# Optimization experiments

Hardware: AMD Instinct MI355X
Metric: run time of the kernel (lower is better)

The kernel has to match this reference:

```python
import jax, jax.numpy as jnp
import numpy as np

B, L, D = 4, 1024, 256
H, HD, W = 8, 64, 3


def setup_inputs() -> dict:
    key = jax.random.key(0)
    ks = jax.random.split(key, 5)
    return {
        'x': jax.random.normal(ks[0], (B, L, D), dtype=jnp.float32),
        'Wq': jax.random.normal(ks[1], (D, H * HD), dtype=jnp.float32) * 0.05,
        'bq': jnp.zeros((H, 1, 1, HD), dtype=jnp.float32),
        'Wk': jax.random.normal(ks[2], (D, H * HD), dtype=jnp.float32) * 0.05,
        'bk': jnp.zeros((H, 1, 1, HD), dtype=jnp.float32),
        'Wv': jax.random.normal(ks[3], (D, H), dtype=jnp.float32) * 0.05,
        'pe': jax.random.normal(ks[4], (L, D), dtype=jnp.float32) * 0.05,
    }


def reference(x, Wq, bq, Wk, bk, Wv, pe):
    b, l, d = x.shape
    h, hd = bq.shape[0], bq.shape[-1]
    xpe = x + pe  # learned positional encoding added for Q and K only
    # tf.split over axis 3 into h heads + concat axis 0 == reshape then head-major transpose
    q = (xpe @ Wq).reshape(b, l, h, hd).transpose(2, 0, 1, 3) + bq  # [H,B,L,hd]
    k = (xpe @ Wk).reshape(b, l, h, hd).transpose(2, 0, 1, 3) + bk  # [H,B,L,hd]
    v = jax.nn.sigmoid(x @ Wv).transpose(2, 0, 1)  # [H,B,L]
    att = jnp.einsum('hbqd,hbkd->hbqk', q, k) / jnp.sqrt(jnp.asarray(hd, x.dtype))
    att = jax.nn.softmax(att, axis=-1)  # [H,B,L,L]
    # band_part(0,-1) + diag_part(k=(0,L-1)) + transpose + reverse(-2,-1) is
    # equivalent to: out[.., jp, dist] = att[.., n-dist, n] with n = L-1-jp, masked n-dist>=0
    jp = jnp.arange(l)
    n = l - 1 - jp                      # reversed position index, [L]
    m = n[:, None] - jp[None, :]        # row (query) index per (pos, distance), [L,L]
    valid = m >= 0
    g = att[:, :, jnp.clip(m, 0), n[:, None]]  # gather diagonals -> [H,B,L,L]
    a = jnp.where(valid, g, jnp.asarray(0, x.dtype)) * v[:, :, :, None]
    # avg pool over the distance (last) axis, window W, stride 1, SAME,
    # TF AvgPool excludes padding from the count
    ssum = jax.lax.reduce_window(a, 0.0, jax.lax.add, (1, 1, 1, W), (1, 1, 1, 1), 'SAME')
    cnt = jax.lax.reduce_window(jnp.ones((l,), a.dtype), 0.0, jax.lax.add, (W,), (1,), 'SAME')
    a = ssum / cnt  # [H,B,L,L]
    # global_mode: permute to [B, pos, dist, H] and sum over positions
    return a.transpose(1, 2, 3, 0).sum(axis=1)  # [B, L, H]
```

## Files before the change

kernel.cpp:

```cpp
#include <hip/hip_runtime.h>
#include <hip/hip_bf16.h>
#include <math.h>

#define B 4
#define L 1024
#define D 256
#define H 8
#define HD 64

#define KB_OFF  1048576
#define VR_OFF  2097152
#define TP_OFF  (VR_OFF + 32768)
#define XP_OFF  (TP_OFF + 1048576)
#define WT_OFF  (XP_OFF + 524288)

typedef short short8 __attribute__((ext_vector_type(8)));
typedef float f32x16 __attribute__((ext_vector_type(16)));

__device__ __forceinline__ unsigned short f2bf(float f) {
  __hip_bfloat16 h = __float2bfloat16(f);
  return *reinterpret_cast<unsigned short*>(&h);
}

__global__ __launch_bounds__(256) void prep_wx_kernel(
    const float* __restrict__ x, const float* __restrict__ Wq,
    const float* __restrict__ Wk, const float* __restrict__ Wv,
    const float* __restrict__ pe, float* __restrict__ ws)
{
  const int tid = threadIdx.x;
  if (blockIdx.x < 32) {
    __shared__ float lds[32][257];
    const int c0 = blockIdx.x * 32;
    const float* W = (c0 < 512) ? Wq : Wk;
    const int cc = c0 & 511;
    const int c = tid & 31, dd = tid >> 5;
    for (int d0 = 0; d0 < 256; d0 += 8)
      lds[c][d0 + dd] = W[(d0 + dd) * 512 + cc + c];
    __syncthreads();
    __hip_bfloat16* WT = (__hip_bfloat16*)(ws + WT_OFF);
    for (int cl = 0; cl < 32; ++cl)
      WT[(c0 + cl) * 256 + tid] = __float2bfloat16(lds[cl][tid]);
    return;
  }

  __shared__ float xs[8][257];
  const int r0 = (blockIdx.x - 32) * 8;
  __hip_bfloat16* XP = (__hip_bfloat16*)(ws + XP_OFF);
  for (int idx = tid; idx < 2048; idx += 256) {
    int rr = idx >> 8, c = idx & 255;
    int gr = r0 + rr, l = gr & 1023;
    float xv = x[gr * 256 + c];
    xs[rr][c] = xv;
    XP[gr * 256 + c] = __float2bfloat16(xv + pe[l * 256 + c]);
  }
  __syncthreads();
  {
    int rr = tid >> 5, h = (tid >> 2) & 7, t4 = tid & 3;
    float acc = 0.f;
    const int d0 = t4 << 6;
#pragma unroll 16
    for (int d = 0; d < 64; ++d) acc += xs[rr][d0 + d] * Wv[(d0 + d) * 8 + h];
    acc += __shfl_down(acc, 1, 4);
    acc += __shfl_down(acc, 2, 4);
    if (t4 == 0) {
      float v = 1.f / (1.f + __expf(-acc));
      int gr = r0 + rr;
      int b = gr >> 10, l = gr & 1023;
      ws[VR_OFF + (h * 4 + b) * 1024 + (1023 - l)] = v;
    }
  }
}

__global__ __launch_bounds__(256) void qkgemm_kernel(float* __restrict__ ws,
    const float* __restrict__ bq, const float* __restrict__ bk)
{
  const int tid = threadIdx.x;
  const int w = tid >> 6, lane = tid & 63;
  const int wid = blockIdx.x * 4 + w;
  const int lt = wid & 127;
  const int cp = wid >> 7;

  const __hip_bfloat16* XP = (const __hip_bfloat16*)(ws + XP_OFF);
  const __hip_bfloat16* WT = (const __hip_bfloat16*)(ws + WT_OFF);

  const int ln = (lt << 5) + (lane & 31);
  const int dlo = (lane >> 5) << 3;
  const int ca = (cp << 6) + (lane & 31);
  const __hip_bfloat16* xr = XP + ln * 256 + dlo;
  const __hip_bfloat16* ar = WT + ca * 256 + dlo;
  const __hip_bfloat16* br = ar + (32 * 256);

  f32x16 acca = {0.f,0.f,0.f,0.f,0.f,0.f,0.f,0.f,0.f,0.f,0.f,0.f,0.f,0.f,0.f,0.f};
  f32x16 accb = {0.f,0.f,0.f,0.f,0.f,0.f,0.f,0.f,0.f,0.f,0.f,0.f,0.f,0.f,0.f,0.f};
#pragma unroll
  for (int k = 0; k < 16; ++k) {
    short8 bf  = *(const short8*)(xr + k * 16);
    short8 afa = *(const short8*)(ar + k * 16);
    short8 afb = *(const short8*)(br + k * 16);
    acca = __builtin_amdgcn_mfma_f32_32x32x16_bf16(afa, bf, acca, 0, 0, 0);
    accb = __builtin_amdgcn_mfma_f32_32x32x16_bf16(afb, bf, accb, 0, 0, 0);
  }

  const int b = ln >> 10, l = ln & 1023;
  const int hq = cp & 7;
  const int hi4 = (lane >> 5) << 2;
  const float* bias = (cp < 8) ? bq : bk;
  const int cbase = hq << 6;
  __hip_bfloat16* base = (__hip_bfloat16*)ws + ((cp < 8) ? 0 : (size_t)KB_OFF * 2);
  __hip_bfloat16* dst = base + ((((size_t)(hq * 4 + b) << 10) + l) << 6);

#pragma unroll
  for (int q = 0; q < 4; ++q) {
    int hd0 = (q << 3) + hi4;
    float4 bv = *(const float4*)(bias + cbase + hd0);
    ushort4 pk;
    pk.x = f2bf(acca[4 * q + 0] + bv.x);
    pk.y = f2bf(acca[4 * q + 1] + bv.y);
    pk.z = f2bf(acca[4 * q + 2] + bv.z);
    pk.w = f2bf(acca[4 * q + 3] + bv.w);
    *(ushort4*)(dst + hd0) = pk;

    int hd1 = hd0 + 32;
    float4 bw = *(const float4*)(bias + cbase + hd1);
    ushort4 pk2;
    pk2.x = f2bf(accb[4 * q + 0] + bw.x);
    pk2.y = f2bf(accb[4 * q + 1] + bw.y);
    pk2.z = f2bf(accb[4 * q + 2] + bw.z);
    pk2.w = f2bf(accb[4 * q + 3] + bw.w);
    *(ushort4*)(dst + hd1) = pk2;
  }
}

__global__ __launch_bounds__(256) void attn_kernel(float* __restrict__ ws)
{
  __shared__ float V[4][64][17];
  __shared__ float Tb[4][1056];
  __shared__ float smerge[4][32];
  const int tid = threadIdx.x;
  const int w = tid >> 6, lane = tid & 63;
  const int i = blockIdx.x;
  const int hb = i & 31;
  const int qt = i >> 5;

  for (int idx = tid; idx < 4 * 1056; idx += 256) (&Tb[0][0])[idx] = 0.f;

  const __hip_bfloat16* Qb = (const __hip_bfloat16*)ws + ((size_t)hb << 16);
  const __hip_bfloat16* Kb = (const __hip_bfloat16*)(ws + KB_OFF) + ((size_t)hb << 16);
  const float* __restrict__ vr = ws + VR_OFF + (hb << 10);

  const int qrow = (qt << 5) + (lane & 31);
  const int dlo = (lane >> 5) << 3;
  const int coff = (lane >> 5) << 2;

  const __hip_bfloat16* qr = Qb + (qrow << 6) + dlo;
  short8 qf0 = *(const short8*)(qr);
  short8 qf1 = *(const short8*)(qr + 16);
  short8 qf2 = *(const short8*)(qr + 32);
  short8 qf3 = *(const short8*)(qr + 48);

#define GLOADK(kt, kf)                                                        \
  {                                                                           \
    const __hip_bfloat16* kr_ = Kb + ((((kt) << 5) + (lane & 31)) << 6) + dlo;\
    kf[0] = *(const short8*)(kr_);                                            \
    kf[1] = *(const short8*)(kr_ + 16);                                       \
    kf[2] = *(const short8*)(kr_ + 32);                                       \
    kf[3] = *(const short8*)(kr_ + 48);                                       \
  }

  float sp0 = 0.f, sp1 = 0.f, sp2 = 0.f, sp3 = 0.f;
#pragma unroll
  for (int t = 0; t < 2; ++t) {
    const int kt0 = w + (t << 2);
    short8 kA[4], kB[4], kC[4], kD[4];
    GLOADK(kt0, kA);
    GLOADK(kt0 + 8, kB);
    GLOADK(kt0 + 16, kC);
    GLOADK(kt0 + 24, kD);
    f32x16 aA = {0.f,0.f,0.f,0.f,0.f,0.f,0.f,0.f,0.f,0.f,0.f,0.f,0.f,0.f,0.f,0.f};
    f32x16 aB = {0.f,0.f,0.f,0.f,0.f,0.f,0.f,0.f,0.f,0.f,0.f,0.f,0.f,0.f,0.f,0.f};
    f32x16 aC = {0.f,0.f,0.f,0.f,0.f,0.f,0.f,0.f,0.f,0.f,0.f,0.f,0.f,0.f,0.f,0.f};
    f32x16 aD = {0.f,0.f,0.f,0.f,0.f,0.f,0.f,0.f,0.f,0.f,0.f,0.f,0.f,0.f,0.f,0.f};
#pragma unroll
    for (int s = 0; s < 4; ++s) {
      short8 qs = (s == 0) ? qf0 : (s == 1) ? qf1 : (s == 2) ? qf2 : qf3;
      aA = __builtin_amdgcn_mfma_f32_32x32x16_bf16(kA[s], qs, aA, 0, 0, 0);
      aB = __builtin_amdgcn_mfma_f32_32x32x16_bf16(kB[s], qs, aB, 0, 0, 0);
      aC = __builtin_amdgcn_mfma_f32_32x32x16_bf16(kC[s], qs, aC, 0, 0, 0);
      aD = __builtin_amdgcn_mfma_f32_32x32x16_bf16(kD[s], qs, aD, 0, 0, 0);
    }
#pragma unroll
    for (int r = 0; r < 16; ++r) {
      sp0 += __expf(aA[r] * 0.125f);
      sp1 += __expf(aB[r] * 0.125f);
      sp2 += __expf(aC[r] * 0.125f);
      sp3 += __expf(aD[r] * 0.125f);
    }
  }
  float s_part = (sp0 + sp1) + (sp2 + sp3);
  s_part += __shfl_xor(s_part, 32);
  if (lane < 32) smerge[w][lane] = s_part;
  __syncthreads();
  const int q = lane & 31;
  const float inv = 1.f / (smerge[0][q] + smerge[1][q] + smerge[2][q] + smerge[3][q]);

#define FLUSH(dt_, acc_)                                                      \
  {                                                                           \
    const int kt_ = qt + (dt_);                                               \
    const float* vb_ = vr + (kt_ << 5) + coff;                                \
    float4 v0_ = *(const float4*)(vb_);                                       \
    float4 v1_ = *(const float4*)(vb_ + 8);                                   \
    float4 v2_ = *(const float4*)(vb_ + 16);                                  \
    float4 v3_ = *(const float4*)(vb_ + 24);                                  \
    _Pragma("unroll")                                                         \
    for (int r = 0; r < 16; ++r) {                                            \
      float vv_ = (r < 4) ? (&v0_.x)[r] : (r < 8) ? (&v1_.x)[r - 4]           \
                : (r < 12) ? (&v2_.x)[r - 8] : (&v3_.x)[r - 12];              \
      V[w][lane][r] = __expf(acc_[r] * 0.125f) * vv_ * inv;                   \
    }                                                                         \
    float accg_ = 0.f;                                                        \
    _Pragma("unroll")                                                         \
    for (int hi = 0; hi < 2; ++hi)                                            \
      _Pragma("unroll")                                                       \
      for (int r = 0; r < 16; ++r) {                                          \
        int l_ = (hi << 2) + (r & 3) + ((r >> 2) << 3) + 31 - lane;           \
        if (l_ >= 0 && l_ < 32) accg_ += V[w][(hi << 5) + l_][r];             \
      }                                                                       \
    Tb[w][((dt_) << 5) + lane] = accg_;                                       \
  }

  const int dtmax = 31 - qt;
  for (int dt = w; dt <= dtmax; dt += 8) {
    const int dt2 = dt + 4;
    const bool has2 = (dt2 <= dtmax);
    const int kta = qt + dt;
    const int ktb = qt + (has2 ? dt2 : dt);
    short8 ka[4], kb[4];
    GLOADK(kta, ka);
    GLOADK(ktb, kb);
    f32x16 acca = {0.f,0.f,0.f,0.f,0.f,0.f,0.f,0.f,0.f,0.f,0.f,0.f,0.f,0.f,0.f,0.f};
    f32x16 accb = {0.f,0.f,0.f,0.f,0.f,0.f,0.f,0.f,0.f,0.f,0.f,0.f,0.f,0.f,0.f,0.f};
    acca = __builtin_amdgcn_mfma_f32_32x32x16_bf16(ka[0], qf0, acca, 0, 0, 0);
    accb = __builtin_amdgcn_mfma_f32_32x32x16_bf16(kb[0], qf0, accb, 0, 0, 0);
    acca = __builtin_amdgcn_mfma_f32_32x32x16_bf16(ka[1], qf1, acca, 0, 0, 0);
    accb = __builtin_amdgcn_mfma_f32_32x32x16_bf16(kb[1], qf1, accb, 0, 0, 0);
    acca = __builtin_amdgcn_mfma_f32_32x32x16_bf16(ka[2], qf2, acca, 0, 0, 0);
    accb = __builtin_amdgcn_mfma_f32_32x32x16_bf16(kb[2], qf2, accb, 0, 0, 0);
    acca = __builtin_amdgcn_mfma_f32_32x32x16_bf16(ka[3], qf3, acca, 0, 0, 0);
    accb = __builtin_amdgcn_mfma_f32_32x32x16_bf16(kb[3], qf3, accb, 0, 0, 0);
    FLUSH(dt, acca);
    if (has2) FLUSH(dt2, accb);
  }
  __syncthreads();

  float* dst = ws + TP_OFF + (((size_t)hb << 5) + qt) * 1024;
  for (int idx = tid; idx < 1024; idx += 256)
    dst[idx] = Tb[0][idx + 31] + Tb[1][idx + 31] + Tb[2][idx + 31] + Tb[3][idx + 31];
}

__global__ __launch_bounds__(256) void out_kernel(const float* __restrict__ ws,
                                                  float* __restrict__ out)
{
  __shared__ float s[130];
  const int tid = threadIdx.x;
  const int i = blockIdx.x;
  const int hb = i & 31;
  const int jc = i >> 5;
  const int j0 = jc << 7;
  const float* TP = ws + TP_OFF + ((size_t)hb << 15);

  if (tid < 130) {
    int j = j0 + tid - 1;
    float acc = 0.f;
    if (j >= 0 && j < 1024) {
#pragma unroll 8
      for (int qt = 0; qt < 32; ++qt) acc += TP[(qt << 10) + j];
    }
    s[tid] = acc;
  }
  __syncthreads();
  if (tid < 128) {
    int j = j0 + tid;
    float cnt = (j == 0 || j == 1023) ? 2.f : 3.f;
    float v = (s[tid] + s[tid + 1] + s[tid + 2]) / cnt;
    int h = hb >> 2, b = hb & 3;
    out[(((b << 10) + j) << 3) + h] = v;
  }
}

extern "C" void kernel_launch(void* const* d_in, const int* in_sizes, int n_in,
                              void* d_out, int out_size, void* d_ws, size_t ws_size,
                              hipStream_t stream)
{
  const float* x  = (const float*)d_in[0];
  const float* Wq = (const float*)d_in[1];
  const float* bq = (const float*)d_in[2];
  const float* Wk = (const float*)d_in[3];
  const float* bk = (const float*)d_in[4];
  const float* Wv = (const float*)d_in[5];
  const float* pe = (const float*)d_in[6];
  float* ws = (float*)d_ws;
  float* out = (float*)d_out;

  prep_wx_kernel<<<dim3(544), dim3(256), 0, stream>>>(x, Wq, Wk, Wv, pe, ws);
  qkgemm_kernel<<<dim3(512), dim3(256), 0, stream>>>(ws, bq, bk);
  attn_kernel<<<dim3(1024), dim3(256), 0, stream>>>(ws);
  out_kernel<<<dim3(256), dim3(256), 0, stream>>>(ws, out);
}
```

Measured before the change: 72.58 us.

## Replace LDS diagonal gather with wave shuffles and write compact per-diagonal partials

The attention kernel no longer stages exp-scaled probabilities in shared memory for the anti-diagonal reduction. It uses cross-lane shuffles instead, and drops the large zeroed Tb buffer and the final block-wide merge. Each wave now writes a compact 64-wide partial per (head-batch, diagonal tile, query tile) straight to global memory. The output kernel then sums only the two relevant diagonal tiles over their valid query tiles. This removes LDS traffic, a barrier and the dense 1024-wide per-tile writes, in exchange for more shuffles and a different global access pattern in the out kernel.

```diff
diff --git a/kernel.cpp b/kernel.cpp
--- a/kernel.cpp
+++ b/kernel.cpp
@@ -10,8 +10,8 @@
 
 #define KB_OFF  1048576
 #define VR_OFF  2097152
-#define TP_OFF  (VR_OFF + 32768)
-#define XP_OFF  (TP_OFF + 1048576)
+#define DP_OFF  (VR_OFF + 32768)
+#define XP_OFF  (DP_OFF + 2097152)
 #define WT_OFF  (XP_OFF + 524288)
 
 typedef short short8 __attribute__((ext_vector_type(8)));
@@ -133,16 +133,12 @@
 
 __global__ __launch_bounds__(256) void attn_kernel(float* __restrict__ ws)
 {
-  __shared__ float V[4][64][17];
-  __shared__ float Tb[4][1056];
   __shared__ float smerge[4][32];
   const int tid = threadIdx.x;
   const int w = tid >> 6, lane = tid & 63;
   const int i = blockIdx.x;
   const int hb = i & 31;
   const int qt = i >> 5;
-
-  for (int idx = tid; idx < 4 * 1056; idx += 256) (&Tb[0][0])[idx] = 0.f;
 
   const __hip_bfloat16* Qb = (const __hip_bfloat16*)ws + ((size_t)hb << 16);
   const __hip_bfloat16* Kb = (const __hip_bfloat16*)(ws + KB_OFF) + ((size_t)hb << 16);
@@ -211,21 +207,24 @@
     float4 v1_ = *(const float4*)(vb_ + 8);                                   \
     float4 v2_ = *(const float4*)(vb_ + 16);                                  \
     float4 v3_ = *(const float4*)(vb_ + 24);                                  \
+    float p_[16];                                                             \
     _Pragma("unroll")                                                         \
     for (int r = 0; r < 16; ++r) {                                            \
       float vv_ = (r < 4) ? (&v0_.x)[r] : (r < 8) ? (&v1_.x)[r - 4]           \
                 : (r < 12) ? (&v2_.x)[r - 8] : (&v3_.x)[r - 12];              \
-      V[w][lane][r] = __expf(acc_[r] * 0.125f) * vv_ * inv;                   \
+      p_[r] = __expf(acc_[r] * 0.125f) * vv_ * inv;                           \
     }                                                                         \
     float accg_ = 0.f;                                                        \
     _Pragma("unroll")                                                         \
     for (int hi = 0; hi < 2; ++hi)                                            \
       _Pragma("unroll")                                                       \
       for (int r = 0; r < 16; ++r) {                                          \
-        int l_ = (hi << 2) + (r & 3) + ((r >> 2) << 3) + 31 - lane;           \
-        if (l_ >= 0 && l_ < 32) accg_ += V[w][(hi << 5) + l_][r];             \
+        const int km_ = (hi << 2) + (r & 3) + ((r >> 2) << 3);                \
+        int src_ = ((hi << 5) + km_ + 31 - lane) & 63;                        \
+        float g_ = __shfl(p_[r], src_);                                       \
+        if (km_ <= lane && km_ >= lane - 31) accg_ += g_;                     \
       }                                                                       \
-    Tb[w][((dt_) << 5) + lane] = accg_;                                       \
+    ws[DP_OFF + ((((hb << 5) + (dt_)) << 5) + qt) * 64 + lane] = accg_;       \
   }
 
   const int dtmax = 31 - qt;
@@ -250,11 +249,6 @@
     FLUSH(dt, acca);
     if (has2) FLUSH(dt2, accb);
   }
-  __syncthreads();
-
-  float* dst = ws + TP_OFF + (((size_t)hb << 5) + qt) * 1024;
-  for (int idx = tid; idx < 1024; idx += 256)
-    dst[idx] = Tb[0][idx + 31] + Tb[1][idx + 31] + Tb[2][idx + 31] + Tb[3][idx + 31];
 }
 
 __global__ __launch_bounds__(256) void out_kernel(const float* __restrict__ ws,
@@ -266,14 +260,24 @@
   const int hb = i & 31;
   const int jc = i >> 5;
   const int j0 = jc << 7;
-  const float* TP = ws + TP_OFF + ((size_t)hb << 15);
+  const float* DP = ws + DP_OFF + ((size_t)hb << 16);
 
   if (tid < 130) {
-    int j = j0 + tid - 1;
+    int jj = j0 + tid - 1;
     float acc = 0.f;
-    if (j >= 0 && j < 1024) {
-#pragma unroll 8
-      for (int qt = 0; qt < 32; ++qt) acc += TP[(qt << 10) + j];
+    if (jj >= 0 && jj < 1024) {
+      int dthi = (jj + 31) >> 5;
+#pragma unroll
+      for (int cand = 0; cand < 2; ++cand) {
+        int dt = dthi - cand;
+        if (dt < 0 || dt > 31) continue;
+        int idx = jj - (dt << 5) + 31;
+        if (idx < 0 || idx > 63) continue;
+        const float* base = DP + (dt << 11) + idx;
+        int nq = 32 - dt;
+        for (int qc = 0; qc < nq; ++qc)
+          acc += base[qc << 6];
+      }
     }
     s[tid] = acc;
   }
```

Result: slower. 86.24 us (+18.8%).
